# Performance work log

Measured on AMD Instinct MI355X. Metric: run time of the kernel, lower is better.

## Reference

```python
import jax, jax.numpy as jnp
import numpy as np

N, T, INPUT_DIM, HIDDEN_DIM = 8, 4096, 128, 128


def setup_inputs() -> dict:
    key = jax.random.key(0)
    k_h, k_wq, k_bq, k_wk, k_bk = jax.random.split(key, 5)
    s = 1.0 / np.sqrt(INPUT_DIM)
    return {
        "H": jax.random.normal(k_h, (N, T, INPUT_DIM), dtype=jnp.float32),
        "Wq": jax.random.uniform(k_wq, (INPUT_DIM, HIDDEN_DIM), jnp.float32, -s, s),
        "bq": jax.random.uniform(k_bq, (HIDDEN_DIM,), jnp.float32, -s, s),
        "Wk": jax.random.uniform(k_wk, (INPUT_DIM, HIDDEN_DIM), jnp.float32, -s, s),
        "bk": jax.random.uniform(k_bk, (HIDDEN_DIM,), jnp.float32, -s, s),
    }


def reference(H, Wq, bq, Wk, bk):
    # Q, K: [N, T, hidden]
    Q = jnp.einsum("ntd,dh->nth", H, Wq) + bq
    K = jnp.einsum("ntd,dh->nth", H, Wk) + bk
    # Faithful quirk: original scales by sqrt(K.transpose(-1,-2).size(-1)) == sqrt(T),
    # NOT sqrt(hidden_dim).
    T_ = H.shape[1]
    scale = 1.0 / jnp.sqrt(jnp.asarray(T_, dtype=H.dtype))
    A = jnp.einsum("nth,nsh->nts", Q, K) * scale  # [N, T, T]
    A = jax.nn.softmax(A, axis=-1)
    # Attention applied directly to H (no V projection), plus residual.
    return jnp.einsum("nts,nsd->ntd", A, H) + H
```

## Files before the change

### kernel.cpp

```cpp
#include <hip/hip_runtime.h>
#include <hip/hip_bf16.h>

typedef __attribute__((ext_vector_type(4))) float f32x4;
typedef __attribute__((ext_vector_type(16))) float f32x16;
typedef __attribute__((ext_vector_type(8))) short s16x8;
typedef unsigned int u32;

#define DEVINL static __device__ __forceinline__

constexpr int TDIM = 4096;
constexpr int DDIM = 128;
constexpr float QSCALE = 1.4426950408889634f / 64.0f;

DEVINL unsigned short f2bf(float f) {
  union { float f; unsigned u; } v; v.f = f;
  unsigned r = v.u + 0x7fffu + ((v.u >> 16) & 1u);
  return (unsigned short)(r >> 16);
}

__global__ void wtrans_kernel(const float* __restrict__ Wq,
                              const float* __restrict__ Wk,
                              unsigned short* __restrict__ Wtq,
                              unsigned short* __restrict__ Wtk) {
  const float* src = blockIdx.x ? Wk : Wq;
  unsigned short* dst = blockIdx.x ? Wtk : Wtq;
  int tid = threadIdx.x;
  for (int k = 0; k < 64; ++k) {
    int e = tid + k * 256;
    int h = e >> 7, d = e & 127;
    dst[h * 128 + d] = f2bf(src[d * 128 + h]);
  }
}

__global__ __launch_bounds__(256) void proj_kernel(
    const float* __restrict__ H, const float* __restrict__ bq,
    const float* __restrict__ bk, const unsigned short* __restrict__ Wtq,
    const unsigned short* __restrict__ Wtk, char* __restrict__ Qb,
    char* __restrict__ Kb, char* __restrict__ Vt) {
  __shared__ __align__(16) unsigned short hs[64][136];
  __shared__ __align__(16) char qs[16384];
  __shared__ __align__(16) char kt[16384];
  __shared__ __align__(16) char vt[16384];
  int b = blockIdx.x;
  int n = b >> 6;
  int t0 = (b & 63) << 6;
  int tid = threadIdx.x;
  const float* Hrow = H + (size_t)(n * TDIM + t0) * DDIM;
#pragma unroll
  for (int k = 0; k < 8; ++k) {
    int e = tid + k * 256;
    int r = e >> 5;
    int c = (e & 31) << 2;
    f32x4 v = *(const f32x4*)(Hrow + r * DDIM + c);
    unsigned short bf[4] = {f2bf(v.x), f2bf(v.y), f2bf(v.z), f2bf(v.w)};
    unsigned short* p = &hs[r][c];
    p[0] = bf[0]; p[1] = bf[1]; p[2] = bf[2]; p[3] = bf[3];
#pragma unroll
    for (int j = 0; j < 4; ++j) {
      int d = c + j;
      int byte = ((d >> 1) * 256 + (d & 1) * 128 + r * 2) ^
                 (((d >> 1) & 15) << 4);
      *(unsigned short*)(vt + byte) = bf[j];
    }
  }
  __syncthreads();
  int w = tid >> 6, ln = tid & 63;
  int lm = ln & 15, lg = ln >> 4;
  int m0 = w * 16;
  s16x8 af[4];
#pragma unroll
  for (int kf = 0; kf < 4; ++kf)
    af[kf] = *(const s16x8*)&hs[m0 + lm][kf * 32 + lg * 8];
#pragma unroll
  for (int nt = 0; nt < 8; ++nt) {
    f32x4 acc = {0.f, 0.f, 0.f, 0.f};
#pragma unroll
    for (int kf = 0; kf < 4; ++kf) {
      s16x8 bfr = *(const s16x8*)&Wtq[(nt * 16 + lm) * 128 + kf * 32 + lg * 8];
      acc = __builtin_amdgcn_mfma_f32_16x16x32_bf16(af[kf], bfr, acc, 0, 0, 0);
    }
    int h = nt * 16 + lm;
    float bv = bq[h];
#pragma unroll
    for (int i = 0; i < 4; ++i) {
      int tl = m0 + lg * 4 + i;
      int byte = tl * 256 + ((h * 2) ^ ((tl & 15) << 4));
      *(unsigned short*)(qs + byte) = f2bf((acc[i] + bv) * QSCALE);
    }
  }
#pragma unroll
  for (int nt = 0; nt < 8; ++nt) {
    f32x4 acc = {0.f, 0.f, 0.f, 0.f};
#pragma unroll
    for (int kf = 0; kf < 4; ++kf) {
      s16x8 bfr = *(const s16x8*)&Wtk[(nt * 16 + lm) * 128 + kf * 32 + lg * 8];
      acc = __builtin_amdgcn_mfma_f32_16x16x32_bf16(af[kf], bfr, acc, 0, 0, 0);
    }
    int h = nt * 16 + lm;
    float bv = bk[h];
#pragma unroll
    for (int i = 0; i < 4; ++i) {
      int rl = m0 + lg * 4 + i;
      int byte = rl * 256 + ((h * 2) ^ ((rl & 15) << 4));
      *(unsigned short*)(kt + byte) = f2bf(acc[i] + bv);
    }
  }
  __syncthreads();
  size_t base = (size_t)(n * TDIM + t0) * 256;
  size_t vbase = ((size_t)(n * 64 + (t0 >> 6)) << 14);
#pragma unroll
  for (int k = 0; k < 4; ++k) {
    int off = tid * 16 + k * 4096;
    *(f32x4*)(Qb + base + off) = *(const f32x4*)(qs + off);
    *(f32x4*)(Kb + base + off) = *(const f32x4*)(kt + off);
    *(f32x4*)(Vt + vbase + off) = *(const f32x4*)(vt + off);
  }
}

DEVINL void stage16(const char* g, char* s, int w, int ln) {
#pragma unroll
  for (int j = 0; j < 2; ++j) {
    int off = (w * 2 + j) * 1024;
    __builtin_amdgcn_global_load_lds(
        (const __attribute__((address_space(1))) void*)(g + off + ln * 16),
        (__attribute__((address_space(3))) void*)(s + off), 16, 0, 0);
  }
}

__global__ __launch_bounds__(512, 2) void attn_kernel(
    const char* __restrict__ Qsw, const char* __restrict__ Ksw,
    const char* __restrict__ Vsw, const float* __restrict__ H,
    float* __restrict__ Out) {
  __shared__ __align__(16) char lds[131072];
  int b = blockIdx.x;
  int n = b & 7;
  int q0 = (b >> 3) << 7;
  int tid = threadIdx.x;
  int w = tid >> 6, ln = tid & 63;
  int q32 = ln & 31, hi = ln >> 5;
  int ws = w & 3;
  int st = w >> 2;
  int qrow = q0 + ws * 32;
  int swz = (q32 & 15) << 4;
  int dpl = q32 >> 1;
  int vswz = dpl << 4;
  int dphalf = (q32 & 1) * 128;

  const char* Kn0 = Ksw + (size_t)n * (TDIM * 256);
  const char* Kn1 = Kn0 + 2048 * 256;
  const char* Vn0 = Vsw + (size_t)n * (64 * 16384);
  const char* Vn1 = Vn0 + (size_t)32 * 16384;

  const char* Qn = Qsw + (size_t)(n * TDIM + qrow + q32) * 256;
  s16x8 qf[8];
#pragma unroll
  for (int d = 0; d < 8; ++d)
    qf[d] = *(const s16x8*)(Qn + ((d * 32 + hi * 16) ^ swz));

  f32x16 o[4];
#pragma unroll
  for (int dt = 0; dt < 4; ++dt) o[dt] = (f32x16)0.0f;
  float lsum = 0.f;

  stage16(Kn0, lds + 0, w, ln);
  stage16(Kn1, lds + 32768, w, ln);
  stage16(Vn0, lds + 65536, w, ln);
  stage16(Vn1, lds + 98304, w, ln);
  __syncthreads();

  for (int it = 0; it < 32; ++it) {
    int c = it & 1;
    if (it < 31) {
      int p2 = c ^ 1;
      size_t go = (size_t)(it + 1) * 16384;
      stage16(Kn0 + go, lds + p2 * 16384, w, ln);
      stage16(Kn1 + go, lds + 32768 + p2 * 16384, w, ln);
      stage16(Vn0 + go, lds + 65536 + p2 * 16384, w, ln);
      stage16(Vn1 + go, lds + 98304 + p2 * 16384, w, ln);
    }
    const char* kb = lds + st * 32768 + c * 16384;
    const char* vb = lds + 65536 + st * 32768 + c * 16384;

    f32x16 s0 = (f32x16)0.0f, s1 = (f32x16)0.0f;
    __builtin_amdgcn_s_setprio(1);
#pragma unroll
    for (int d = 0; d < 8; ++d) {
      int col = d * 32 + hi * 16;
      s16x8 ka0 = *(const s16x8*)(kb + ((q32 * 256 + col) ^ swz));
      s16x8 ka1 = *(const s16x8*)(kb + (((q32 + 32) * 256 + col) ^ swz));
      s0 = __builtin_amdgcn_mfma_f32_32x32x16_bf16(ka0, qf[d], s0, 0, 0, 0);
      s1 = __builtin_amdgcn_mfma_f32_32x32x16_bf16(ka1, qf[d], s1, 0, 0, 0);
    }
    __builtin_amdgcn_s_setprio(0);

    f32x16 p0, p1;
#pragma unroll
    for (int r = 0; r < 16; ++r) {
      p0[r] = __builtin_amdgcn_exp2f(s0[r]);
      p1[r] = __builtin_amdgcn_exp2f(s1[r]);
    }
    float ls = 0.f;
#pragma unroll
    for (int r = 0; r < 16; ++r) ls += p0[r] + p1[r];
    lsum += ls;

    s16x8 pa[4];
#pragma unroll
    for (int kt = 0; kt < 2; ++kt) {
      u32 P2[8];
#pragma unroll
      for (int r = 0; r < 8; ++r) {
        float e0 = kt ? p1[2 * r] : p0[2 * r];
        float e1 = kt ? p1[2 * r + 1] : p0[2 * r + 1];
        asm("v_cvt_pk_bf16_f32 %0, %1, %2" : "=v"(P2[r]) : "v"(e0), "v"(e1));
      }
#pragma unroll
      for (int b2 = 0; b2 < 2; ++b2) {
        u32 a0 = P2[b2 * 4 + 0], c0 = P2[b2 * 4 + 2];
        u32 a1 = P2[b2 * 4 + 1], c1 = P2[b2 * 4 + 3];
        asm("v_permlane32_swap_b32 %0, %1" : "+v"(a0), "+v"(c0));
        asm("v_permlane32_swap_b32 %0, %1" : "+v"(a1), "+v"(c1));
        union { u32 u[4]; s16x8 v; } pk;
        pk.u[0] = a0; pk.u[1] = a1; pk.u[2] = c0; pk.u[3] = c1;
        pa[kt * 2 + b2] = pk.v;
      }
    }

    __builtin_amdgcn_s_setprio(1);
#pragma unroll
    for (int ks = 0; ks < 4; ++ks) {
      int colv = dphalf + ks * 32 + hi * 16;
#pragma unroll
      for (int dt = 0; dt < 4; ++dt) {
        int dp = dt * 16 + dpl;
        s16x8 vv = *(const s16x8*)(vb + ((dp * 256 + colv) ^ vswz));
        o[dt] = __builtin_amdgcn_mfma_f32_32x32x16_bf16(pa[ks], vv, o[dt], 0, 0, 0);
      }
    }
    __builtin_amdgcn_s_setprio(0);
    __syncthreads();
  }

  if (w >= 4) {
    char* dst = lds + (w - 4) * 16896;
#pragma unroll
    for (int dt = 0; dt < 4; ++dt)
#pragma unroll
      for (int c4 = 0; c4 < 4; ++c4) {
        f32x4 ch = {o[dt][c4 * 4 + 0], o[dt][c4 * 4 + 1],
                    o[dt][c4 * 4 + 2], o[dt][c4 * 4 + 3]};
        *(f32x4*)(dst + ((dt * 4 + c4) * 64 + ln) * 16) = ch;
      }
    *(float*)(dst + 16384 + ln * 4) = lsum;
  }
  __syncthreads();
  if (w < 4) {
    const char* src = lds + w * 16896;
#pragma unroll
    for (int dt = 0; dt < 4; ++dt)
#pragma unroll
      for (int c4 = 0; c4 < 4; ++c4) {
        f32x4 ch = *(const f32x4*)(src + ((dt * 4 + c4) * 64 + ln) * 16);
        o[dt][c4 * 4 + 0] += ch.x; o[dt][c4 * 4 + 1] += ch.y;
        o[dt][c4 * 4 + 2] += ch.z; o[dt][c4 * 4 + 3] += ch.w;
      }
    lsum += *(const float*)(src + 16384 + ln * 4);
    u32 la = __builtin_bit_cast(u32, lsum), lb = la;
    asm("v_permlane32_swap_b32 %0, %1" : "+v"(la), "+v"(lb));
    float ltot = __builtin_bit_cast(float, la) + __builtin_bit_cast(float, lb);
    float invl = 1.0f / ltot;
    if (hi == 0) *(float*)(lds + 67584 + w * 128 + q32 * 4) = invl;
  }
  __syncthreads();
  if (w < 4) {
    const float* Hn = H + (size_t)n * TDIM * DDIM;
    float* On = Out + (size_t)n * TDIM * DDIM;
    float iv[16];
#pragma unroll
    for (int r = 0; r < 16; ++r) {
      int qr = (r & 3) + 8 * (r >> 2) + 4 * hi;
      iv[r] = *(const float*)(lds + 67584 + w * 128 + qr * 4);
    }
#pragma unroll
    for (int dt = 0; dt < 4; ++dt)
#pragma unroll
      for (int r = 0; r < 16; ++r) {
        int qr = (r & 3) + 8 * (r >> 2) + 4 * hi;
        size_t idx = (size_t)(qrow + qr) * DDIM + dt * 32 + q32;
        On[idx] = o[dt][r] * iv[r] + Hn[idx];
      }
  }
}

extern "C" void kernel_launch(void* const* d_in, const int* in_sizes, int n_in,
                              void* d_out, int out_size, void* d_ws, size_t ws_size,
                              hipStream_t stream) {
  const float* H  = (const float*)d_in[0];
  const float* Wq = (const float*)d_in[1];
  const float* bq = (const float*)d_in[2];
  const float* Wk = (const float*)d_in[3];
  const float* bk = (const float*)d_in[4];
  float* Out = (float*)d_out;
  char* ws = (char*)d_ws;
  unsigned short* Wtq = (unsigned short*)(ws);
  unsigned short* Wtk = (unsigned short*)(ws + 32768);
  char* Qb = ws + 65536;
  char* Kb = ws + 65536 + 8388608;
  char* Vt = ws + 65536 + 2 * 8388608;

  wtrans_kernel<<<2, 256, 0, stream>>>(Wq, Wk, Wtq, Wtk);
  proj_kernel<<<512, 256, 0, stream>>>(H, bq, bk, Wtq, Wtk, Qb, Kb, Vt);
  attn_kernel<<<256, 512, 0, stream>>>(Qb, Kb, Vt, H, Out);
}
```

Before: 108.5 us.

## Load K fragments directly from global memory in MFMA layout, stage only V in LDS

The projection kernel now writes K in a fragment-ordered layout, so each lane can read its MFMA operand with one contiguous 16-byte global load. The attention kernel drops K staging through LDS, which halves LDS use (131 KB down to about 68 KB) and removes the K async copies. The intent is to cut LDS traffic and capacity pressure. In exchange, every K read now goes to global/L2 memory with latency exposed inside the QK loop and no prefetch. The setprio hints around QK are also removed.

```diff
diff --git a/kernel.cpp b/kernel.cpp
--- a/kernel.cpp
+++ b/kernel.cpp
@@ -96,13 +96,13 @@
       s16x8 bfr = *(const s16x8*)&Wtk[(nt * 16 + lm) * 128 + kf * 32 + lg * 8];
       acc = __builtin_amdgcn_mfma_f32_16x16x32_bf16(af[kf], bfr, acc, 0, 0, 0);
     }
-    int h = nt * 16 + lm;
-    float bv = bk[h];
+    int hip2 = ((lm >> 3) & 1) * 32;
+    int jj = lm & 7;
 #pragma unroll
     for (int i = 0; i < 4; ++i) {
       int rl = m0 + lg * 4 + i;
-      int byte = rl * 256 + ((h * 2) ^ ((rl & 15) << 4));
-      *(unsigned short*)(kt + byte) = f2bf(acc[i] + bv);
+      int byte = (rl >> 5) * 8192 + nt * 1024 + (hip2 + (rl & 31)) * 16 + jj * 2;
+      *(unsigned short*)(kt + byte) = f2bf(acc[i] + bk[nt * 16 + lm]);
     }
   }
   __syncthreads();
@@ -131,7 +131,7 @@
     const char* __restrict__ Qsw, const char* __restrict__ Ksw,
     const char* __restrict__ Vsw, const float* __restrict__ H,
     float* __restrict__ Out) {
-  __shared__ __align__(16) char lds[131072];
+  __shared__ __align__(16) char lds[69632];
   int b = blockIdx.x;
   int n = b & 7;
   int q0 = (b >> 3) << 7;
@@ -146,8 +146,7 @@
   int vswz = dpl << 4;
   int dphalf = (q32 & 1) * 128;
 
-  const char* Kn0 = Ksw + (size_t)n * (TDIM * 256);
-  const char* Kn1 = Kn0 + 2048 * 256;
+  const char* Kn = Ksw + (size_t)n * (TDIM * 256);
   const char* Vn0 = Vsw + (size_t)n * (64 * 16384);
   const char* Vn1 = Vn0 + (size_t)32 * 16384;
 
@@ -162,10 +161,8 @@
   for (int dt = 0; dt < 4; ++dt) o[dt] = (f32x16)0.0f;
   float lsum = 0.f;
 
-  stage16(Kn0, lds + 0, w, ln);
-  stage16(Kn1, lds + 32768, w, ln);
-  stage16(Vn0, lds + 65536, w, ln);
-  stage16(Vn1, lds + 98304, w, ln);
+  stage16(Vn0, lds + 0, w, ln);
+  stage16(Vn1, lds + 32768, w, ln);
   __syncthreads();
 
   for (int it = 0; it < 32; ++it) {
@@ -173,25 +170,20 @@
     if (it < 31) {
       int p2 = c ^ 1;
       size_t go = (size_t)(it + 1) * 16384;
-      stage16(Kn0 + go, lds + p2 * 16384, w, ln);
-      stage16(Kn1 + go, lds + 32768 + p2 * 16384, w, ln);
-      stage16(Vn0 + go, lds + 65536 + p2 * 16384, w, ln);
-      stage16(Vn1 + go, lds + 98304 + p2 * 16384, w, ln);
-    }
-    const char* kb = lds + st * 32768 + c * 16384;
-    const char* vb = lds + 65536 + st * 32768 + c * 16384;
+      stage16(Vn0 + go, lds + p2 * 16384, w, ln);
+      stage16(Vn1 + go, lds + 32768 + p2 * 16384, w, ln);
+    }
+    const char* vb = lds + st * 32768 + c * 16384;
+    const char* kt = Kn + ((size_t)(st * 32 + it) << 14);
 
     f32x16 s0 = (f32x16)0.0f, s1 = (f32x16)0.0f;
-    __builtin_amdgcn_s_setprio(1);
 #pragma unroll
     for (int d = 0; d < 8; ++d) {
-      int col = d * 32 + hi * 16;
-      s16x8 ka0 = *(const s16x8*)(kb + ((q32 * 256 + col) ^ swz));
-      s16x8 ka1 = *(const s16x8*)(kb + (((q32 + 32) * 256 + col) ^ swz));
+      s16x8 ka0 = *(const s16x8*)(kt + d * 1024 + ln * 16);
+      s16x8 ka1 = *(const s16x8*)(kt + 8192 + d * 1024 + ln * 16);
       s0 = __builtin_amdgcn_mfma_f32_32x32x16_bf16(ka0, qf[d], s0, 0, 0, 0);
       s1 = __builtin_amdgcn_mfma_f32_32x32x16_bf16(ka1, qf[d], s1, 0, 0, 0);
     }
-    __builtin_amdgcn_s_setprio(0);
 
     f32x16 p0, p1;
 #pragma unroll
@@ -206,12 +198,12 @@
 
     s16x8 pa[4];
 #pragma unroll
-    for (int kt = 0; kt < 2; ++kt) {
+    for (int kt2 = 0; kt2 < 2; ++kt2) {
       u32 P2[8];
 #pragma unroll
       for (int r = 0; r < 8; ++r) {
-        float e0 = kt ? p1[2 * r] : p0[2 * r];
-        float e1 = kt ? p1[2 * r + 1] : p0[2 * r + 1];
+        float e0 = kt2 ? p1[2 * r] : p0[2 * r];
+        float e1 = kt2 ? p1[2 * r + 1] : p0[2 * r + 1];
         asm("v_cvt_pk_bf16_f32 %0, %1, %2" : "=v"(P2[r]) : "v"(e0), "v"(e1));
       }
 #pragma unroll
@@ -222,7 +214,7 @@
         asm("v_permlane32_swap_b32 %0, %1" : "+v"(a1), "+v"(c1));
         union { u32 u[4]; s16x8 v; } pk;
         pk.u[0] = a0; pk.u[1] = a1; pk.u[2] = c0; pk.u[3] = c1;
-        pa[kt * 2 + b2] = pk.v;
+        pa[kt2 * 2 + b2] = pk.v;
       }
     }
 
```

New measurement: 126.1 us. 16.2% more time.
